# Performance work log

Measured on AMD Instinct MI355X. Metric: run time of the kernel, lower is better.

## Reference

```python
import jax, jax.numpy as jnp
import numpy as np

B, N, C_IN, C_OUT, K = 2, 2048, 64, 128, 3
SCALE = 12.0  # spread points over ~12^3 unit voxels (voxel_size = 1.0 in the module)


def setup_inputs() -> dict:
    key = jax.random.key(0)
    k1, k2, k3 = jax.random.split(key, 3)
    points = jax.random.uniform(k1, (B, N, 3), dtype=jnp.float32) * SCALE
    features = jax.random.normal(k2, (B, N, C_IN), dtype=jnp.float32)
    # kaiming-uniform-ish init for weight viewed as (K^3*Cin, Cout)
    fan_in = K * K * K * C_IN
    bound = np.sqrt(6.0 / fan_in)
    weight = jax.random.uniform(k3, (K, K, K, C_IN, C_OUT), dtype=jnp.float32,
                                minval=-bound, maxval=bound)
    bias = jnp.zeros((C_OUT,), dtype=jnp.float32)
    return {"points": points, "features": features, "weight": weight, "bias": bias}


def reference(points, features, weight, bias):
    """Sparse 3D conv over a unit voxel grid.

    For each point i, every point j whose voxel index differs by an offset
    within the KxKxK stencil contributes features[j] @ weight[rel_offset].
    Vectorized as: per-offset boolean match matrix (B,N,N) -> masked
    feature aggregation -> one GEMM with that offset's (Cin,Cout) kernel slice.
    """
    k = weight.shape[0]
    c = k // 2
    # torch's .long() truncates toward zero; jnp astype(int32) does the same for floats
    vox = points.astype(jnp.int32)  # (B, N, 3)
    out = jnp.zeros(features.shape[:2] + (weight.shape[-1],), dtype=features.dtype)
    for oi in range(k):
        for oj in range(k):
            for ok in range(k):
                off = jnp.array([oi - c, oj - c, ok - c], dtype=jnp.int32)
                target = vox + off  # voxel that neighbor j must occupy for center i
                # mask[b, i, j] = all(vox[b, j] == vox[b, i] + off)
                mask = jnp.all(vox[:, None, :, :] == target[:, :, None, :], axis=-1)
                agg = jnp.einsum('bij,bjc->bic', mask.astype(features.dtype), features)
                out = out + agg @ weight[oi, oj, ok]  # (B,N,Cin)@(Cin,Cout)
    return out + bias
```

## Files before the change

### kernel.cpp

```cpp
#include <hip/hip_runtime.h>

#define BATCH 2
#define NPTS  2048
#define CIN   64
#define COUT  128
#define GD    14
#define GD2   (GD*GD)
#define NCELL (GD*GD*GD)
#define M     (BATCH*NPTS)
#define VOXF  (BATCH*NCELL*CIN)
#define WTEL  (27*COUT*CIN)

typedef __bf16 bf16x8 __attribute__((ext_vector_type(8)));
typedef float  f32x4  __attribute__((ext_vector_type(4)));
typedef unsigned short us8 __attribute__((ext_vector_type(8)));

__device__ __forceinline__ unsigned short f2bf(float f) {
    unsigned u = __builtin_bit_cast(unsigned, f);
    return (unsigned short)((u + 0x7FFFu + ((u >> 16) & 1u)) >> 16);
}

__global__ __launch_bounds__(256) void k_init(const float* __restrict__ points,
                                              const float* __restrict__ weight,
                                              float* __restrict__ voxgrid,
                                              int* __restrict__ cellid,
                                              unsigned short* __restrict__ wT) {
    int idx = blockIdx.x * 256 + threadIdx.x;
    if (idx < VOXF/4) ((float4*)voxgrid)[idx] = make_float4(0.f, 0.f, 0.f, 0.f);
    if (idx < M) {
        int vx = (int)points[idx*3 + 0];
        int vy = (int)points[idx*3 + 1];
        int vz = (int)points[idx*3 + 2];
        cellid[idx] = (vx + 1)*GD2 + (vy + 1)*GD + (vz + 1);
    }
    if (idx < WTEL) {
        int off = idx >> 13;
        int rem = idx & 8191;
        int n   = rem >> 6;
        int k   = rem & 63;
        wT[idx] = f2bf(weight[off*8192 + k*128 + n]);
    }
}

__global__ __launch_bounds__(256) void k_scatter(const float* __restrict__ feat,
                                                 const int* __restrict__ cellid,
                                                 float* __restrict__ voxgrid) {
    int idx = blockIdx.x * 256 + threadIdx.x;
    int g   = idx >> 6;
    int cin = idx & 63;
    int b   = g >> 11;
    atomicAdd(&voxgrid[((size_t)b*NCELL + cellid[g])*CIN + cin], feat[idx]);
}

__global__ __launch_bounds__(256) void k_gemm(const float* __restrict__ voxgrid,
                                              const int* __restrict__ cellid,
                                              const unsigned short* __restrict__ wT,
                                              const float* __restrict__ bias,
                                              float* __restrict__ out) {
    static constexpr int DELTA[27] = {
        -211,-210,-209,-197,-196,-195,-183,-182,-181,
         -15, -14, -13,  -1,   0,   1,  13,  14,  15,
         181, 182, 183, 195, 196, 197, 209, 210, 211 };

    __shared__ unsigned short Abuf[16*72];

    const int t   = threadIdx.x;
    const int g0  = blockIdx.x * 16;
    const int b   = g0 >> 11;

    const int row = t >> 4;
    const int c4  = (t & 15) * 4;
    const int cell = cellid[g0 + row];
    const float* aptr = voxgrid + ((size_t)b*NCELL + cell)*CIN + c4;

    const int l   = t & 63;
    const int w   = t >> 6;
    const int q   = l >> 4;
    const int col = l & 15;
    const int n0  = blockIdx.y * 64 + w * 16;
    const unsigned short* wt0 = wT + (size_t)(n0 + col)*CIN + q*8;
    const unsigned short* abase = &Abuf[(l & 15)*72 + q*8];

    f32x4 acc = {0.f, 0.f, 0.f, 0.f};

    float4 v  = *(const float4*)(aptr + DELTA[0]*CIN);
    us8    b0 = *(const us8*)(wt0);
    us8    b1 = *(const us8*)(wt0 + 32);

    #pragma unroll
    for (int oo = 0; oo < 27; ++oo) {
        __syncthreads();
        ushort4 pk;
        pk.x = f2bf(v.x); pk.y = f2bf(v.y); pk.z = f2bf(v.z); pk.w = f2bf(v.w);
        *(ushort4*)&Abuf[row*72 + c4] = pk;
        __syncthreads();

        if (oo < 26) {
            v  = *(const float4*)(aptr + DELTA[oo+1]*CIN);
        }
        us8 b0n, b1n;
        if (oo < 26) {
            b0n = *(const us8*)(wt0 + (oo+1)*8192);
            b1n = *(const us8*)(wt0 + (oo+1)*8192 + 32);
        }

        us8 a0 = *(const us8*)(abase);
        us8 a1 = *(const us8*)(abase + 32);
        acc = __builtin_amdgcn_mfma_f32_16x16x32_bf16(
                  __builtin_bit_cast(bf16x8, a0), __builtin_bit_cast(bf16x8, b0), acc, 0, 0, 0);
        acc = __builtin_amdgcn_mfma_f32_16x16x32_bf16(
                  __builtin_bit_cast(bf16x8, a1), __builtin_bit_cast(bf16x8, b1), acc, 0, 0, 0);

        if (oo < 26) { b0 = b0n; b1 = b1n; }
    }

    const float bs = bias[n0 + col];
    #pragma unroll
    for (int r = 0; r < 4; ++r) {
        out[(size_t)(g0 + q*4 + r)*COUT + n0 + col] = acc[r] + bs;
    }
}

extern "C" void kernel_launch(void* const* d_in, const int* in_sizes, int n_in,
                              void* d_out, int out_size, void* d_ws, size_t ws_size,
                              hipStream_t stream) {
    (void)in_sizes; (void)n_in; (void)out_size; (void)ws_size;
    const float* points   = (const float*)d_in[0];
    const float* features = (const float*)d_in[1];
    const float* weight   = (const float*)d_in[2];
    const float* bias     = (const float*)d_in[3];
    float* out = (float*)d_out;

    float*          voxgrid = (float*)d_ws;
    int*            cellid  = (int*)((char*)d_ws + (size_t)VOXF*4);
    unsigned short* wTp     = (unsigned short*)((char*)d_ws + (size_t)VOXF*4 + (size_t)M*4);

    k_init<<<(WTEL + 255)/256, 256, 0, stream>>>(points, weight, voxgrid, cellid, wTp);
    k_scatter<<<(M*CIN + 255)/256, 256, 0, stream>>>(features, cellid, voxgrid);
    dim3 grid(M/16, 2, 1);
    k_gemm<<<grid, 256, 0, stream>>>(voxgrid, cellid, wTp, bias, out);
}
```

Baseline: 80.76 us.

## Pre-pack voxel grid to bf16 and stream GEMM operands directly into MFMA registers

Adds a pack kernel that converts the fp32 voxel grid to bf16 once, so the GEMM loads bf16 A fragments straight from global memory. This removes the per-offset LDS staging, conversion and two barriers per iteration, and replaces them with a 3-deep register prefetch of A and B. The weight transpose now goes through an LDS tile in 27 blocks instead of strided per-element reads. Grid zeroing moves to hipMemsetAsync, and the per-point base offset is precomputed. The cost is one extra kernel launch and an extra pass over the grid, with hardcoded workspace offsets.

```diff
diff --git a/kernel.cpp b/kernel.cpp
--- a/kernel.cpp
+++ b/kernel.cpp
@@ -22,38 +22,60 @@
 
 __global__ __launch_bounds__(256) void k_init(const float* __restrict__ points,
                                               const float* __restrict__ weight,
-                                              float* __restrict__ voxgrid,
-                                              int* __restrict__ cellid,
+                                              int* __restrict__ abase,
                                               unsigned short* __restrict__ wT) {
-    int idx = blockIdx.x * 256 + threadIdx.x;
-    if (idx < VOXF/4) ((float4*)voxgrid)[idx] = make_float4(0.f, 0.f, 0.f, 0.f);
-    if (idx < M) {
-        int vx = (int)points[idx*3 + 0];
-        int vy = (int)points[idx*3 + 1];
-        int vz = (int)points[idx*3 + 2];
-        cellid[idx] = (vx + 1)*GD2 + (vy + 1)*GD + (vz + 1);
-    }
-    if (idx < WTEL) {
-        int off = idx >> 13;
-        int rem = idx & 8191;
-        int n   = rem >> 6;
-        int k   = rem & 63;
-        wT[idx] = f2bf(weight[off*8192 + k*128 + n]);
+    const int t = threadIdx.x;
+    if (blockIdx.x < 27) {
+        const int off = blockIdx.x;
+        __shared__ unsigned short lds[128*65 + 64];
+        const float* wsrc = weight + off*8192;
+        #pragma unroll
+        for (int i = 0; i < 32; ++i) {
+            const int s = t + i*256;
+            const int k = s >> 7, n = s & 127;
+            lds[n*65 + k] = f2bf(wsrc[k*128 + n]);
+        }
+        __syncthreads();
+        unsigned short* wdst = wT + off*8192;
+        #pragma unroll
+        for (int i = 0; i < 32; ++i) {
+            const int s = t + i*256;
+            const int n = s >> 6, k = s & 63;
+            wdst[n*64 + k] = lds[n*65 + k];
+        }
+    } else {
+        const int g = (blockIdx.x - 27)*256 + t;
+        const int vx = (int)points[g*3 + 0];
+        const int vy = (int)points[g*3 + 1];
+        const int vz = (int)points[g*3 + 2];
+        const int cell = (vx + 1)*GD2 + (vy + 1)*GD + (vz + 1);
+        abase[g] = ((g >> 11)*NCELL + cell)*CIN;
     }
 }
 
 __global__ __launch_bounds__(256) void k_scatter(const float* __restrict__ feat,
-                                                 const int* __restrict__ cellid,
+                                                 const int* __restrict__ abase,
                                                  float* __restrict__ voxgrid) {
-    int idx = blockIdx.x * 256 + threadIdx.x;
-    int g   = idx >> 6;
-    int cin = idx & 63;
-    int b   = g >> 11;
-    atomicAdd(&voxgrid[((size_t)b*NCELL + cellid[g])*CIN + cin], feat[idx]);
+    const int idx = blockIdx.x * 256 + threadIdx.x;
+    const int g   = idx >> 6;
+    const int cin = idx & 63;
+    atomicAdd(&voxgrid[abase[g] + cin], feat[idx]);
 }
 
-__global__ __launch_bounds__(256) void k_gemm(const float* __restrict__ voxgrid,
-                                              const int* __restrict__ cellid,
+__global__ __launch_bounds__(256) void k_pack(const float* __restrict__ voxgrid,
+                                              unsigned short* __restrict__ voxbf) {
+    const int idx = blockIdx.x * 256 + threadIdx.x;
+    if (idx >= VOXF/8) return;
+    const float4 v0 = ((const float4*)voxgrid)[idx*2 + 0];
+    const float4 v1 = ((const float4*)voxgrid)[idx*2 + 1];
+    us8 p;
+    p[0] = f2bf(v0.x); p[1] = f2bf(v0.y); p[2] = f2bf(v0.z); p[3] = f2bf(v0.w);
+    p[4] = f2bf(v1.x); p[5] = f2bf(v1.y); p[6] = f2bf(v1.z); p[7] = f2bf(v1.w);
+    *(us8*)(voxbf + idx*8) = p;
+}
+
+__global__ __launch_bounds__(256) void k_gemm(const unsigned short* __restrict__ voxbf,
+                                              const int* __restrict__ abase,
                                               const unsigned short* __restrict__ wT,
                                               const float* __restrict__ bias,
                                               float* __restrict__ out) {
@@ -62,56 +84,45 @@
          -15, -14, -13,  -1,   0,   1,  13,  14,  15,
          181, 182, 183, 195, 196, 197, 209, 210, 211 };
 
-    __shared__ unsigned short Abuf[16*72];
-
     const int t   = threadIdx.x;
-    const int g0  = blockIdx.x * 16;
-    const int b   = g0 >> 11;
-
-    const int row = t >> 4;
-    const int c4  = (t & 15) * 4;
-    const int cell = cellid[g0 + row];
-    const float* aptr = voxgrid + ((size_t)b*NCELL + cell)*CIN + c4;
-
     const int l   = t & 63;
     const int w   = t >> 6;
     const int q   = l >> 4;
     const int col = l & 15;
-    const int n0  = blockIdx.y * 64 + w * 16;
-    const unsigned short* wt0 = wT + (size_t)(n0 + col)*CIN + q*8;
-    const unsigned short* abase = &Abuf[(l & 15)*72 + q*8];
+    const int g0  = blockIdx.x * 16;
+    const int n0  = (blockIdx.y * 4 + w) * 16;
+
+    const int rowoff = abase[g0 + col];
+    const unsigned short* arow = voxbf + rowoff + q*8;
+    const unsigned short* wtp  = wT + (size_t)(n0 + col)*CIN + q*8;
 
     f32x4 acc = {0.f, 0.f, 0.f, 0.f};
 
-    float4 v  = *(const float4*)(aptr + DELTA[0]*CIN);
-    us8    b0 = *(const us8*)(wt0);
-    us8    b1 = *(const us8*)(wt0 + 32);
+    us8 A0[3], A1[3], B0[3], B1[3];
+    #pragma unroll
+    for (int p = 0; p < 3; ++p) {
+        const int d = DELTA[p]*CIN;
+        A0[p] = *(const us8*)(arow + d);
+        A1[p] = *(const us8*)(arow + d + 32);
+        B0[p] = *(const us8*)(wtp + p*8192);
+        B1[p] = *(const us8*)(wtp + p*8192 + 32);
+    }
 
     #pragma unroll
     for (int oo = 0; oo < 27; ++oo) {
-        __syncthreads();
-        ushort4 pk;
-        pk.x = f2bf(v.x); pk.y = f2bf(v.y); pk.z = f2bf(v.z); pk.w = f2bf(v.w);
-        *(ushort4*)&Abuf[row*72 + c4] = pk;
-        __syncthreads();
-
-        if (oo < 26) {
-            v  = *(const float4*)(aptr + DELTA[oo+1]*CIN);
+        const int s = oo % 3;
+        const us8 a0 = A0[s], a1 = A1[s], b0 = B0[s], b1 = B1[s];
+        if (oo + 3 < 27) {
+            const int d = DELTA[oo+3]*CIN;
+            A0[s] = *(const us8*)(arow + d);
+            A1[s] = *(const us8*)(arow + d + 32);
+            B0[s] = *(const us8*)(wtp + (oo+3)*8192);
+            B1[s] = *(const us8*)(wtp + (oo+3)*8192 + 32);
         }
-        us8 b0n, b1n;
-        if (oo < 26) {
-            b0n = *(const us8*)(wt0 + (oo+1)*8192);
-            b1n = *(const us8*)(wt0 + (oo+1)*8192 + 32);
-        }
-
-        us8 a0 = *(const us8*)(abase);
-        us8 a1 = *(const us8*)(abase + 32);
         acc = __builtin_amdgcn_mfma_f32_16x16x32_bf16(
                   __builtin_bit_cast(bf16x8, a0), __builtin_bit_cast(bf16x8, b0), acc, 0, 0, 0);
         acc = __builtin_amdgcn_mfma_f32_16x16x32_bf16(
                   __builtin_bit_cast(bf16x8, a1), __builtin_bit_cast(bf16x8, b1), acc, 0, 0, 0);
-
-        if (oo < 26) { b0 = b0n; b1 = b1n; }
     }
 
     const float bs = bias[n0 + col];
@@ -131,12 +142,16 @@
     const float* bias     = (const float*)d_in[3];
     float* out = (float*)d_out;
 
-    float*          voxgrid = (float*)d_ws;
-    int*            cellid  = (int*)((char*)d_ws + (size_t)VOXF*4);
-    unsigned short* wTp     = (unsigned short*)((char*)d_ws + (size_t)VOXF*4 + (size_t)M*4);
+    char* ws = (char*)d_ws;
+    float*          voxgrid = (float*)ws;
+    int*            abase   = (int*)(ws + 1404928);
+    unsigned short* wTp     = (unsigned short*)(ws + 1404928 + 16384);
+    unsigned short* voxbf   = (unsigned short*)(ws + 1404928 + 16384 + 442368);
 
-    k_init<<<(WTEL + 255)/256, 256, 0, stream>>>(points, weight, voxgrid, cellid, wTp);
-    k_scatter<<<(M*CIN + 255)/256, 256, 0, stream>>>(features, cellid, voxgrid);
+    hipMemsetAsync(voxgrid, 0, (size_t)VOXF*4, stream);
+    k_init<<<43, 256, 0, stream>>>(points, weight, abase, wTp);
+    k_scatter<<<(M*CIN)/256, 256, 0, stream>>>(features, abase, voxgrid);
+    k_pack<<<(VOXF/8 + 255)/256, 256, 0, stream>>>(voxgrid, voxbf);
     dim3 grid(M/16, 2, 1);
-    k_gemm<<<grid, 256, 0, stream>>>(voxgrid, cellid, wTp, bias, out);
+    k_gemm<<<grid, 256, 0, stream>>>(voxbf, abase, wTp, bias, out);
 }
```

Measured after the change: 94.87 us. 1.17x slower.
